# Performance work log

Hardware: AMD Instinct MI355X
Metric: run time of the kernel (lower is better)

The kernel has to match this reference:

```python
import jax, jax.numpy as jnp
import numpy as np

B, S, VOCAB, E, H, T = 256, 512, 50000, 256, 256, 32
PAD = VOCAB - 1  # mask = sentences != vocab_size - 1 in the original


def setup_inputs() -> dict:
    key = jax.random.key(0)
    ks = jax.random.split(key, 16)
    lengths = jnp.sort(jax.random.randint(ks[0], (B,), S // 2, S + 1))[::-1]
    lengths = lengths.at[0].set(S)  # sorted descending, max length present
    sentences = jax.random.randint(ks[1], (B, S), 0, VOCAB - 1)
    pos = jnp.arange(S)
    sentences = jnp.where(pos[None, :] < lengths[:, None], sentences, PAD)
    tags = jax.random.randint(ks[2], (B, S), 0, T)
    sc = jnp.float32(0.1)
    p = lambda k, shp: jax.random.normal(k, shp, jnp.float32) * sc
    return {
        'embed_table': p(ks[3], (VOCAB + 1, E)),
        'W_ih_f': p(ks[4], (4 * H, E)), 'W_hh_f': p(ks[5], (4 * H, H)),
        'b_ih_f': p(ks[6], (4 * H,)), 'b_hh_f': p(ks[7], (4 * H,)),
        'W_ih_b': p(ks[8], (4 * H, E)), 'W_hh_b': p(ks[9], (4 * H, H)),
        'b_ih_b': p(ks[10], (4 * H,)), 'b_hh_b': p(ks[11], (4 * H,)),
        'W_out': p(ks[12], (T, 2 * H)), 'b_out': p(ks[13], (T,)),
        'transition': jax.random.normal(ks[14], (T, T), jnp.float32),
        'sentences': sentences, 'tags': tags, 'sen_lengths': lengths,
    }


def _run_lstm(x_sbe, W_ih, W_hh, b_ih, b_hh):
    # x_sbe: [S, B, E]; torch gate order i, f, g, o
    Bsz, Hd = x_sbe.shape[1], W_hh.shape[1]
    gx = jnp.einsum('sbe,ge->sbg', x_sbe, W_ih) + b_ih + b_hh  # precompute input gates
    def step(carry, g):
        h, c = carry
        g = g + h @ W_hh.T
        i, f, gg, o = jnp.split(g, 4, axis=-1)
        c = jax.nn.sigmoid(f) * c + jax.nn.sigmoid(i) * jnp.tanh(gg)
        h = jax.nn.sigmoid(o) * jnp.tanh(c)
        return (h, c), h
    h0 = jnp.zeros((Bsz, Hd), x_sbe.dtype)
    _, hs = jax.lax.scan(step, (h0, h0), gx)
    return hs  # [S, B, H]


def _forward(embed_table, W_ih_f, W_hh_f, b_ih_f, b_hh_f,
             W_ih_b, W_hh_b, b_ih_b, b_hh_b, W_out, b_out, transition,
             sentences, tags, sen_lengths):
    mask = sentences != PAD                      # [B, S]
    x = embed_table[sentences]                   # [B, S, E]
    pos = jnp.arange(S)
    valid = pos[None, :] < sen_lengths[:, None]  # [B, S]
    # per-sequence reversal index (packed-sequence-faithful backward direction)
    idx = jnp.where(valid, sen_lengths[:, None] - 1 - pos[None, :], pos[None, :])
    h_f = _run_lstm(x.transpose(1, 0, 2), W_ih_f, W_hh_f, b_ih_f, b_hh_f).transpose(1, 0, 2)
    x_rev = jnp.take_along_axis(x, idx[:, :, None], axis=1)
    h_b = _run_lstm(x_rev.transpose(1, 0, 2), W_ih_b, W_hh_b, b_ih_b, b_hh_b).transpose(1, 0, 2)
    h_b = jnp.take_along_axis(h_b, idx[:, :, None], axis=1)
    h = jnp.concatenate([h_f, h_b], -1) * valid[:, :, None]  # pad_packed pads with zeros
    emit = h @ W_out.T + b_out                   # [B, S, T]; dropout is identity (eval)
    # ---- CRF negative log-likelihood ----
    fmask = mask.astype(emit.dtype)
    real = jnp.take_along_axis(emit, tags[:, :, None], axis=2)[..., 0]  # [B, S]
    real = real.at[:, 1:].add(transition[tags[:, :-1], tags[:, 1:]])
    real_score = (real * fmask).sum(axis=1)      # [B]
    def crf_step(alpha, inp):
        e_i, m_i = inp                           # [B, T], [B]
        scores = alpha[:, :, None] + transition[None, :, :] + e_i[:, None, :]
        new = jax.nn.logsumexp(scores, axis=1)
        return jnp.where(m_i[:, None], new, alpha), None
    alpha0 = emit[:, 0]                          # [B, T]
    xs = (emit[:, 1:].transpose(1, 0, 2), mask[:, 1:].T)
    alpha, _ = jax.lax.scan(crf_step, alpha0, xs)
    log_z = jax.nn.logsumexp(alpha, axis=1)      # [B]
    return -(real_score - log_z)                 # per-example loss [B]


def reference(embed_table, W_ih_f, W_hh_f, b_ih_f, b_hh_f,
              W_ih_b, W_hh_b, b_ih_b, b_hh_b, W_out, b_out, transition,
              sentences, tags, sen_lengths):
    return _forward(embed_table, W_ih_f, W_hh_f, b_ih_f, b_hh_f,
                    W_ih_b, W_hh_b, b_ih_b, b_hh_b, W_out, b_out, transition,
                    sentences, tags, sen_lengths)
```

## Files before the change

### kernel.cpp

```cpp
#include <hip/hip_runtime.h>
#include <hip/hip_bf16.h>


typedef __bf16 bf16x8 __attribute__((ext_vector_type(8)));
typedef float f32x4 __attribute__((ext_vector_type(4)));
typedef unsigned int uint4v __attribute__((ext_vector_type(4)));

__device__ __forceinline__ unsigned short f2bf(float f) {
  union { float f; unsigned int u; } v; v.f = f;
  unsigned int r = v.u + 0x7fffu + ((v.u >> 16) & 1u);
  return (unsigned short)(r >> 16);
}
__device__ __forceinline__ float bf2f(unsigned int lo16) {
  union { unsigned int u; float f; } v; v.u = lo16 << 16;
  return v.f;
}
__device__ __forceinline__ float fsig(float x) {
  float e = __builtin_amdgcn_exp2f(-1.4426950408889634f * x);
  return __builtin_amdgcn_rcpf(1.0f + e);
}
__device__ __forceinline__ float ftanh(float x) {
  float e = __builtin_amdgcn_exp2f(2.8853900817779268f * x);
  return 1.0f - 2.0f * __builtin_amdgcn_rcpf(e + 1.0f);
}

__device__ __forceinline__ void wait_ge(int* p, int target) {
  if (threadIdx.x == 0) {
    while (__hip_atomic_load(p, __ATOMIC_RELAXED, __HIP_MEMORY_SCOPE_AGENT) < target)
      __builtin_amdgcn_s_sleep(2);
    (void)__hip_atomic_load(p, __ATOMIC_ACQUIRE, __HIP_MEMORY_SCOPE_AGENT);
  }
  __syncthreads();
}

__global__ void cvt_weights(const float* __restrict__ wih_f, const float* __restrict__ wih_b,
                            const float* __restrict__ whh_f, const float* __restrict__ whh_b,
                            const float* __restrict__ wo,
                            unsigned short* __restrict__ wih,
                            unsigned char* __restrict__ whh8,
                            unsigned char* __restrict__ wout8,
                            int* __restrict__ flags) {
  if (blockIdx.x == 0 && threadIdx.x < 32) flags[threadIdx.x] = 0;
  int t = blockIdx.x * 256 + threadIdx.x;
  int i = t * 4;
  if (i < 524288) {
    const float* src = (i < 262144) ? wih_f : wih_b;
    f32x4 v = *(const f32x4*)(src + (i & 262143));
    uint2 p;
    p.x = f2bf(v[0]) | ((unsigned int)f2bf(v[1]) << 16);
    p.y = f2bf(v[2]) | ((unsigned int)f2bf(v[3]) << 16);
    *(uint2*)(wih + i) = p;
  } else if (i < 1048576) {
    int k = i - 524288;
    const float* src = (k < 262144) ? whh_f : whh_b;
    f32x4 v = *(const f32x4*)(src + (k & 262143));
    int r = 0;
    r = __builtin_amdgcn_cvt_pk_fp8_f32(v[0], v[1], r, false);
    r = __builtin_amdgcn_cvt_pk_fp8_f32(v[2], v[3], r, true);
    *(unsigned int*)(whh8 + k) = (unsigned int)r;
  } else if (i < 1064960) {
    int k = i - 1048576;
    f32x4 v = *(const f32x4*)(wo + k);
    int r = 0;
    r = __builtin_amdgcn_cvt_pk_fp8_f32(v[0], v[1], r, false);
    r = __builtin_amdgcn_cvt_pk_fp8_f32(v[2], v[3], r, true);
    *(unsigned int*)(wout8 + k) = (unsigned int)r;
  }
}


__device__ void gemm_role(
    const float* __restrict__ emb, const int* __restrict__ sent, const int* __restrict__ lens,
    const unsigned short* __restrict__ wih,
    const float* __restrict__ bih_f, const float* __restrict__ bhh_f,
    const float* __restrict__ bih_b, const float* __restrict__ bhh_b,
    unsigned short* __restrict__ gx, int* flags,
    unsigned short* wtile, float* btile)
{
  int gb = blockIdx.x - 64;
  int tid = threadIdx.x, w = tid >> 6, lane = tid & 63, col = lane & 15, q = lane >> 4;
  int ns = w >> 2, cg = w & 3;
  int prev_chunk = -1;

  for (int idx = gb; idx < 4096; idx += 192) {
    int k = idx >> 8, t = idx & 255;
    if (k != prev_chunk) {
      prev_chunk = k;
      if (k >= 2) wait_ge(&flags[16 + k - 2], 64);
    }
    int dir = t >> 7, r = t & 127;
    int nc = r >> 4, bt = (r >> 2) & 3, ss = r & 3;
    int n0 = nc * 128, bbase = bt * 64;
    int s0 = k * 32, sbase = s0 + ss * 8;

    if (sbase < lens[bbase]) {
      const unsigned short* wsrc = wih + (size_t)dir * 262144;
#pragma unroll
      for (int it = 0; it < 8; it++) {
        int seg = it * 512 + tid;
        int row = seg >> 5, kc = (seg & 31) * 8;
        *(uint4v*)(wtile + row * 264 + kc) = *(const uint4v*)(wsrc + (size_t)(n0 + row) * 256 + kc);
      }
      const float* bi = dir ? bih_b : bih_f;
      const float* bh = dir ? bhh_b : bhh_f;
      if (tid < 128) btile[tid] = bi[n0 + tid] + bh[n0 + tid];
      __syncthreads();

      bf16x8 wf[8][4];
#pragma unroll
      for (int kt = 0; kt < 8; kt++)
#pragma unroll
        for (int nt = 0; nt < 4; nt++)
          wf[kt][nt] = *(const bf16x8*)(wtile + (ns * 64 + nt * 16 + col) * 264 + kt * 32 + q * 8);
      f32x4 bias[4];
#pragma unroll
      for (int nt = 0; nt < 4; nt++)
#pragma unroll
        for (int rr = 0; rr < 4; rr++)
          bias[nt][rr] = btile[ns * 64 + nt * 16 + q * 4 + rr];

      int bidx = bbase + cg * 16 + col;
      int len = lens[bidx];
      const int* srow = sent + bidx * 512;

      for (int i = 0; i < 8; i++) {
        int s = sbase + i;
        int s_eff = dir ? ((s < len) ? (len - 1 - s) : s) : s;
        int token = srow[s_eff];
        const float* ep = emb + (size_t)token * 256;
        bf16x8 xf[8];
#pragma unroll
        for (int kt = 0; kt < 8; kt++) {
          f32x4 a0 = *(const f32x4*)(ep + kt * 32 + q * 8);
          f32x4 a1 = *(const f32x4*)(ep + kt * 32 + q * 8 + 4);
          uint4v pk;
          pk[0] = f2bf(a0[0]) | ((unsigned int)f2bf(a0[1]) << 16);
          pk[1] = f2bf(a0[2]) | ((unsigned int)f2bf(a0[3]) << 16);
          pk[2] = f2bf(a1[0]) | ((unsigned int)f2bf(a1[1]) << 16);
          pk[3] = f2bf(a1[2]) | ((unsigned int)f2bf(a1[3]) << 16);
          xf[kt] = __builtin_bit_cast(bf16x8, pk);
        }
        f32x4 acc[4];
#pragma unroll
        for (int nt = 0; nt < 4; nt++) acc[nt] = bias[nt];
#pragma unroll
        for (int kt = 0; kt < 8; kt++)
#pragma unroll
          for (int nt = 0; nt < 4; nt++)
            acc[nt] = __builtin_amdgcn_mfma_f32_16x16x32_bf16(wf[kt][nt], xf[kt], acc[nt], 0, 0, 0);
        size_t off = (size_t)(k & 1) * 16777216 + (size_t)dir * 8388608
                   + (size_t)(s - s0) * 262144 + (size_t)bidx * 1024 + n0 + ns * 64;
#pragma unroll
        for (int nt = 0; nt < 4; nt++) {
          uint2 pk;
          pk.x = f2bf(acc[nt][0]) | ((unsigned int)f2bf(acc[nt][1]) << 16);
          pk.y = f2bf(acc[nt][2]) | ((unsigned int)f2bf(acc[nt][3]) << 16);
          *(uint2*)(gx + off + nt * 16 + q * 4) = pk;
        }
      }
    }
    __syncthreads();
    if (tid == 0)
      __hip_atomic_fetch_add(&flags[k], 1, __ATOMIC_RELEASE, __HIP_MEMORY_SCOPE_AGENT);
  }
}

__device__ void lstm_role(
    const unsigned short* __restrict__ gx,
    const unsigned char* __restrict__ whh8,
    const unsigned char* __restrict__ wout8,
    const float* __restrict__ bout,
    const int* __restrict__ lens,
    unsigned short* __restrict__ emit_f, unsigned short* __restrict__ emit_b,
    int* flags, unsigned char (*hb4)[16 * 264])
{
  int bx = blockIdx.x;
  int dir = bx & 1, grp = bx >> 1, b0 = grp * 8;
  int tid = threadIdx.x, w = tid >> 6, lane = tid & 63, col = lane & 15, q = lane >> 4;
  int maxlen = lens[b0];
  int bcl = b0 + col; if (bcl > 255) bcl = 255;
  int mylen = lens[bcl];

  const unsigned char* whb = whh8 + (size_t)dir * 262144;
  long wh[8][8];
#pragma unroll
  for (int kt = 0; kt < 8; kt++)
#pragma unroll
    for (int t = 0; t < 8; t++) {
      int row0 = (t & 3) * 256 + w * 32 + (t >> 2) * 16;
      wh[kt][t] = *(const long*)(whb + (size_t)(row0 + col) * 256 + kt * 32 + q * 8);
    }

  long wo8[8];
  f32x4 bo4 = (f32x4){0.f, 0.f, 0.f, 0.f};
#pragma unroll
  for (int kt = 0; kt < 8; kt++)
    wo8[kt] = *(const long*)(wout8 + (size_t)((w & 1) * 16 + col) * 512 + dir * 256 + kt * 32 + q * 8);
  if (dir == 0) {
#pragma unroll
    for (int r = 0; r < 4; r++) bo4[r] = bout[(w & 1) * 16 + q * 4 + r];
  }
  unsigned short* ebase = dir ? emit_b : emit_f;

  float c8[8];
  long hf8[8];
#pragma unroll
  for (int i = 0; i < 8; i++) { c8[i] = 0.f; hf8[i] = 0; }

  for (int c = 0; c < 16; c++) {
    int s0 = c * 32;
    if (s0 < maxlen) {
      wait_ge(&flags[c], 256);
      int send = s0 + 32; if (send > maxlen) send = maxlen;
      const unsigned short* gl = gx + (size_t)(c & 1) * 16777216 + (size_t)dir * 8388608
                                    + (size_t)bcl * 1024 + q * 4;
      uint2 gxr[8];
#pragma unroll
      for (int t = 0; t < 8; t++) {
        int row0 = (t & 3) * 256 + w * 32 + (t >> 2) * 16;
        gxr[t] = *(const uint2*)(gl + row0);
      }

      for (int s = s0; s < send; s++) {
        f32x4 acc[8];
#pragma unroll
        for (int t = 0; t < 8; t++) {
          f32x4 a;
          a[0] = bf2f(gxr[t].x & 0xffffu); a[1] = bf2f(gxr[t].x >> 16);
          a[2] = bf2f(gxr[t].y & 0xffffu); a[3] = bf2f(gxr[t].y >> 16);
          acc[t] = a;
        }
        {
          int snl = (s + 1 < send) ? (s + 1 - s0) : (send - 1 - s0);
          const unsigned short* gn = gl + (size_t)snl * 262144;
#pragma unroll
          for (int t = 0; t < 8; t++) {
            int row0 = (t & 3) * 256 + w * 32 + (t >> 2) * 16;
            gxr[t] = *(const uint2*)(gn + row0);
          }
        }
#pragma unroll
        for (int kt = 0; kt < 8; kt++) {
          long hv8 = hf8[kt];
#pragma unroll
          for (int t = 0; t < 8; t++)
            acc[t] = __builtin_amdgcn_mfma_f32_16x16x32_fp8_fp8(wh[kt][t], hv8, acc[t], 0, 0, 0);
        }
        float hv[8];
#pragma unroll
        for (int a = 0; a < 2; a++)
#pragma unroll
          for (int r = 0; r < 4; r++) {
            float ig = acc[a * 4 + 0][r], fg = acc[a * 4 + 1][r];
            float gg = acc[a * 4 + 2][r], og = acc[a * 4 + 3][r];
            float cn = fsig(fg) * c8[a * 4 + r] + fsig(ig) * ftanh(gg);
            c8[a * 4 + r] = cn;
            hv[a * 4 + r] = fsig(og) * ftanh(cn);
          }
        int par = s & 7;
#pragma unroll
        for (int a = 0; a < 2; a++) {
          int r8 = 0;
          r8 = __builtin_amdgcn_cvt_pk_fp8_f32(hv[a * 4 + 0], hv[a * 4 + 1], r8, false);
          r8 = __builtin_amdgcn_cvt_pk_fp8_f32(hv[a * 4 + 2], hv[a * 4 + 3], r8, true);
          *(unsigned int*)(&hb4[par][col * 264 + w * 32 + a * 16 + q * 4]) = (unsigned int)r8;
        }
        __syncthreads();
#pragma unroll
        for (int kt = 0; kt < 8; kt++)
          hf8[kt] = *(const long*)(&hb4[par][col * 264 + kt * 32 + q * 8]);

        if ((s & 3) == 3 || s == send - 1) {
          int ebeg = s & ~3;
          int e = ebeg + (w >> 1);
          if (e <= s) {
            f32x4 ea = bo4;
#pragma unroll
            for (int kt = 0; kt < 8; kt++) {
              long hbv = *(const long*)(&hb4[e & 7][col * 264 + kt * 32 + q * 8]);
              ea = __builtin_amdgcn_mfma_f32_16x16x32_fp8_fp8(wo8[kt], hbv, ea, 0, 0, 0);
            }
            if (col < 8 && e < mylen) {
              int pos = dir ? (mylen - 1 - e) : e;
              uint2 pk;
              pk.x = f2bf(ea[0]) | ((unsigned int)f2bf(ea[1]) << 16);
              pk.y = f2bf(ea[2]) | ((unsigned int)f2bf(ea[3]) << 16);
              *(uint2*)(ebase + (((size_t)(b0 + col) * 512 + pos) * 32 + (w & 1) * 16 + q * 4)) = pk;
            }
          }
        }
      }
    }
    __syncthreads();
    if (tid == 0)
      __hip_atomic_fetch_add(&flags[16 + c], 1, __ATOMIC_RELEASE, __HIP_MEMORY_SCOPE_AGENT);
  }
}

__global__ __launch_bounds__(512, 2) void fused_persist(
    const float* __restrict__ emb, const int* __restrict__ sent, const int* __restrict__ lens,
    const unsigned short* __restrict__ wih,
    const float* __restrict__ bih_f, const float* __restrict__ bhh_f,
    const float* __restrict__ bih_b, const float* __restrict__ bhh_b,
    unsigned short* __restrict__ gx,
    const unsigned char* __restrict__ whh8, const unsigned char* __restrict__ wout8,
    const float* __restrict__ bout,
    unsigned short* __restrict__ emit_f, unsigned short* __restrict__ emit_b,
    int* flags)
{
  __shared__ __align__(16) unsigned short wtile[128 * 264];
  __shared__ __align__(16) float btile[128];
  __shared__ __align__(16) unsigned char hb4[8][16 * 264];

  if (blockIdx.x < 64) {
    lstm_role(gx, whh8, wout8, bout, lens, emit_f, emit_b, flags, hb4);
  } else {
    gemm_role(emb, sent, lens, wih, bih_f, bhh_f, bih_b, bhh_b, gx, flags, wtile, btile);
  }
}

__global__ __launch_bounds__(64) void crf_kernel(
    const unsigned short* __restrict__ emit_f,
    const unsigned short* __restrict__ emit_b,
    const float* __restrict__ trans, const int* __restrict__ tags,
    const int* __restrict__ lens, float* __restrict__ out) {
  const float LOG2E = 1.4426950408889634f, LN2 = 0.6931471805599453f;
  __shared__ __align__(16) float e_lds[512 * 32];
  int b = blockIdx.x, lane = threadIdx.x;
  int len = lens[b];
  const int* tg = tags + b * 512;

  size_t ebase = (size_t)b * 512 * 32;
  const unsigned short* pf = emit_f + ebase;
  const unsigned short* pb = emit_b + ebase;
  int ng = len * 4;
  for (int g = lane; g < ng; g += 64) {
    uint4v fv = *(const uint4v*)(pf + g * 8);
    uint4v bv = *(const uint4v*)(pb + g * 8);
    f32x4 w0, w1;
#pragma unroll
    for (int k = 0; k < 2; k++) {
      w0[2 * k]     = (bf2f(fv[k] & 0xffffu) + bf2f(bv[k] & 0xffffu)) * LOG2E;
      w0[2 * k + 1] = (bf2f(fv[k] >> 16)     + bf2f(bv[k] >> 16))     * LOG2E;
      w1[2 * k]     = (bf2f(fv[k + 2] & 0xffffu) + bf2f(bv[k + 2] & 0xffffu)) * LOG2E;
      w1[2 * k + 1] = (bf2f(fv[k + 2] >> 16)     + bf2f(bv[k + 2] >> 16))     * LOG2E;
    }
    *(f32x4*)(e_lds + g * 8) = w0;
    *(f32x4*)(e_lds + g * 8 + 4) = w1;
  }
  __syncthreads();

  float rs2 = 0.f, rst = 0.f;
  for (int s = lane; s < len; s += 64) {
    int t1 = tg[s];
    rs2 += e_lds[s * 32 + t1];
    if (s > 0) rst += trans[tg[s - 1] * 32 + t1];
  }
  float rsc = LN2 * rs2 + rst;
#pragma unroll
  for (int m = 32; m; m >>= 1) rsc += __shfl_xor(rsc, m);

  int j = lane & 31, half = lane >> 5, i0 = half * 16;
  float tr2[16];
  int pidx[16];
#pragma unroll
  for (int ii = 0; ii < 16; ii++) {
    tr2[ii] = trans[(i0 + ii) * 32 + j] * LOG2E;
    pidx[ii] = (i0 + ii) << 2;
  }
  const float* ep = e_lds + j;
  float B = ep[0];
  float e_nxt = ep[32];
  for (int s = 1; s < len; s++) {
    float e_cur = e_nxt;
    int sn = (s + 1 < len) ? (s + 1) : s;
    e_nxt = ep[sn * 32];
    float v[16];
#pragma unroll
    for (int ii = 0; ii < 16; ii++)
      v[ii] = __builtin_bit_cast(float, __builtin_amdgcn_ds_bpermute(
                  pidx[ii], __builtin_bit_cast(int, B))) + tr2[ii];
    float a8[8], a4[4], a2[2];
#pragma unroll
    for (int ii = 0; ii < 8; ii++) a8[ii] = fmaxf(v[ii], v[ii + 8]);
#pragma unroll
    for (int ii = 0; ii < 4; ii++) a4[ii] = fmaxf(a8[ii], a8[ii + 4]);
    a2[0] = fmaxf(a4[0], a4[2]); a2[1] = fmaxf(a4[1], a4[3]);
    float m1 = fmaxf(a2[0], a2[1]);
    float m2 = fmaxf(m1, __shfl_xor(m1, 32));
    float x[16];
#pragma unroll
    for (int ii = 0; ii < 16; ii++) x[ii] = __builtin_amdgcn_exp2f(v[ii] - m2);
    float s8[8], s4[4], s2[2];
#pragma unroll
    for (int ii = 0; ii < 8; ii++) s8[ii] = x[ii] + x[ii + 8];
#pragma unroll
    for (int ii = 0; ii < 4; ii++) s4[ii] = s8[ii] + s8[ii + 4];
    s2[0] = s4[0] + s4[2]; s2[1] = s4[1] + s4[3];
    float sum = s2[0] + s2[1];
    sum += __shfl_xor(sum, 32);
    B = m2 + __builtin_amdgcn_logf(sum) + e_cur;
  }
  float mz = B;
#pragma unroll
  for (int m = 16; m; m >>= 1) mz = fmaxf(mz, __shfl_xor(mz, m));
  float sz = __builtin_amdgcn_exp2f(B - mz);
#pragma unroll
  for (int m = 16; m; m >>= 1) sz += __shfl_xor(sz, m);
  float logz = LN2 * (mz + __builtin_amdgcn_logf(sz));
  if (lane == 0) out[b] = logz - rsc;
}

extern "C" void kernel_launch(void* const* d_in, const int* in_sizes, int n_in,
                              void* d_out, int out_size, void* d_ws, size_t ws_size,
                              hipStream_t stream) {
  const float* emb   = (const float*)d_in[0];
  const float* Wih_f = (const float*)d_in[1];
  const float* Whh_f = (const float*)d_in[2];
  const float* bih_f = (const float*)d_in[3];
  const float* bhh_f = (const float*)d_in[4];
  const float* Wih_b = (const float*)d_in[5];
  const float* Whh_b = (const float*)d_in[6];
  const float* bih_b = (const float*)d_in[7];
  const float* bhh_b = (const float*)d_in[8];
  const float* Wout  = (const float*)d_in[9];
  const float* bout  = (const float*)d_in[10];
  const float* trans = (const float*)d_in[11];
  const int* sent = (const int*)d_in[12];
  const int* tags = (const int*)d_in[13];
  const int* lens = (const int*)d_in[14];
  float* out = (float*)d_out;

  char* ws = (char*)d_ws;
  if (ws_size < 87048192ull) return;
  unsigned short* gx      = (unsigned short*)(ws);
  unsigned short* emit_f  = (unsigned short*)(ws + 67108864);
  unsigned short* emit_b  = (unsigned short*)(ws + 75497472);
  unsigned short* wih_bf  = (unsigned short*)(ws + 83886080);
  unsigned char*  whh8    = (unsigned char*)(ws + 84934656);
  unsigned char*  wout8   = (unsigned char*)(ws + 85458944);
  int*            flags   = (int*)(ws + 85475328);

  cvt_weights<<<1040, 256, 0, stream>>>(Wih_f, Wih_b, Whh_f, Whh_b, Wout,
                                        wih_bf, whh8, wout8, flags);
  fused_persist<<<256, 512, 0, stream>>>(
      emb, sent, lens, wih_bf, bih_f, bhh_f, bih_b, bhh_b, gx,
      whh8, wout8, bout, emit_f, emit_b, flags);
  crf_kernel<<<256, 64, 0, stream>>>(emit_f, emit_b, trans, tags, lens, out);
}
```

Before: 1.735 ms.

## Use 16-sequence LSTM blocks with fine-grained per-subchunk producer flags

LSTM blocks now each handle 16 sequences instead of 8, so half as many blocks (32) run the recurrence and more blocks (224) run the input-projection GEMM. The single per-chunk ready flag is replaced by flags per 8-step subchunk, direction and batch tile, so the recurrence can start as soon as its own slice of gx is written. The per-step __syncthreads is replaced by an explicit lgkmcnt wait plus s_barrier. This risks a longer serial recurrence per block, since each block now does twice the columns, and puts more polling traffic on the flags.

```diff
diff --git a/kernel.cpp b/kernel.cpp
--- a/kernel.cpp
+++ b/kernel.cpp
@@ -31,6 +31,10 @@
     (void)__hip_atomic_load(p, __ATOMIC_ACQUIRE, __HIP_MEMORY_SCOPE_AGENT);
   }
   __syncthreads();
+}
+
+__device__ __forceinline__ void lds_barrier() {
+  asm volatile("s_waitcnt lgkmcnt(0)\n\ts_barrier" ::: "memory");
 }
 
 __global__ void cvt_weights(const float* __restrict__ wih_f, const float* __restrict__ wih_b,
@@ -40,7 +44,9 @@
                             unsigned char* __restrict__ whh8,
                             unsigned char* __restrict__ wout8,
                             int* __restrict__ flags) {
-  if (blockIdx.x == 0 && threadIdx.x < 32) flags[threadIdx.x] = 0;
+  if (blockIdx.x == 0) {
+    for (int f = threadIdx.x; f < 544; f += 256) flags[f] = 0;
+  }
   int t = blockIdx.x * 256 + threadIdx.x;
   int i = t * 4;
   if (i < 524288) {
@@ -77,21 +83,21 @@
     unsigned short* __restrict__ gx, int* flags,
     unsigned short* wtile, float* btile)
 {
-  int gb = blockIdx.x - 64;
+  int gb = blockIdx.x - 32;
   int tid = threadIdx.x, w = tid >> 6, lane = tid & 63, col = lane & 15, q = lane >> 4;
   int ns = w >> 2, cg = w & 3;
   int prev_chunk = -1;
 
-  for (int idx = gb; idx < 4096; idx += 192) {
+  for (int idx = gb; idx < 4096; idx += 224) {
     int k = idx >> 8, t = idx & 255;
+    int ss = t >> 6, rest = t & 63;
+    int dir = (rest >> 5) & 1, nc = (rest >> 2) & 7, bt = rest & 3;
     if (k != prev_chunk) {
       prev_chunk = k;
-      if (k >= 2) wait_ge(&flags[16 + k - 2], 64);
+      if (k >= 2) wait_ge(&flags[512 + k - 2], 32);
     }
-    int dir = t >> 7, r = t & 127;
-    int nc = r >> 4, bt = (r >> 2) & 3, ss = r & 3;
     int n0 = nc * 128, bbase = bt * 64;
-    int s0 = k * 32, sbase = s0 + ss * 8;
+    int sbase = k * 32 + ss * 8;
 
     if (sbase < lens[bbase]) {
       const unsigned short* wsrc = wih + (size_t)dir * 262144;
@@ -149,7 +155,7 @@
           for (int nt = 0; nt < 4; nt++)
             acc[nt] = __builtin_amdgcn_mfma_f32_16x16x32_bf16(wf[kt][nt], xf[kt], acc[nt], 0, 0, 0);
         size_t off = (size_t)(k & 1) * 16777216 + (size_t)dir * 8388608
-                   + (size_t)(s - s0) * 262144 + (size_t)bidx * 1024 + n0 + ns * 64;
+                   + (size_t)(s - k * 32) * 262144 + (size_t)bidx * 1024 + n0 + ns * 64;
 #pragma unroll
         for (int nt = 0; nt < 4; nt++) {
           uint2 pk;
@@ -161,7 +167,8 @@
     }
     __syncthreads();
     if (tid == 0)
-      __hip_atomic_fetch_add(&flags[k], 1, __ATOMIC_RELEASE, __HIP_MEMORY_SCOPE_AGENT);
+      __hip_atomic_fetch_add(&flags[k * 32 + ss * 8 + dir * 4 + bt], 1,
+                             __ATOMIC_RELEASE, __HIP_MEMORY_SCOPE_AGENT);
   }
 }
 
@@ -175,10 +182,11 @@
     int* flags, unsigned char (*hb4)[16 * 264])
 {
   int bx = blockIdx.x;
-  int dir = bx & 1, grp = bx >> 1, b0 = grp * 8;
+  int dir = bx & 1, grp = bx >> 1, b0 = grp * 16;
+  int bt = grp >> 2;
   int tid = threadIdx.x, w = tid >> 6, lane = tid & 63, col = lane & 15, q = lane >> 4;
   int maxlen = lens[b0];
-  int bcl = b0 + col; if (bcl > 255) bcl = 255;
+  int bcl = b0 + col;
   int mylen = lens[bcl];
 
   const unsigned char* whb = whh8 + (size_t)dir * 262144;
@@ -210,82 +218,90 @@
   for (int c = 0; c < 16; c++) {
     int s0 = c * 32;
     if (s0 < maxlen) {
-      wait_ge(&flags[c], 256);
-      int send = s0 + 32; if (send > maxlen) send = maxlen;
-      const unsigned short* gl = gx + (size_t)(c & 1) * 16777216 + (size_t)dir * 8388608
-                                    + (size_t)bcl * 1024 + q * 4;
-      uint2 gxr[8];
-#pragma unroll
-      for (int t = 0; t < 8; t++) {
-        int row0 = (t & 3) * 256 + w * 32 + (t >> 2) * 16;
-        gxr[t] = *(const uint2*)(gl + row0);
-      }
-
-      for (int s = s0; s < send; s++) {
-        f32x4 acc[8];
-#pragma unroll
-        for (int t = 0; t < 8; t++) {
-          f32x4 a;
-          a[0] = bf2f(gxr[t].x & 0xffffu); a[1] = bf2f(gxr[t].x >> 16);
-          a[2] = bf2f(gxr[t].y & 0xffffu); a[3] = bf2f(gxr[t].y >> 16);
-          acc[t] = a;
-        }
+      int cend = s0 + 32; if (cend > maxlen) cend = maxlen;
+      const unsigned short* gbase = gx + (size_t)(c & 1) * 16777216 + (size_t)dir * 8388608
+                                       + (size_t)bcl * 1024 + q * 4;
+      for (int ss = 0; ss < 4; ss++) {
+        int sp0 = s0 + ss * 8;
+        if (sp0 >= maxlen) break;
+        int spe = sp0 + 8; if (spe > cend) spe = cend;
+        wait_ge(&flags[c * 32 + ss * 8 + dir * 4 + bt], 8);
+
+        uint2 gxr[8];
         {
-          int snl = (s + 1 < send) ? (s + 1 - s0) : (send - 1 - s0);
-          const unsigned short* gn = gl + (size_t)snl * 262144;
+          const unsigned short* gf = gbase + (size_t)(sp0 - s0) * 262144;
 #pragma unroll
           for (int t = 0; t < 8; t++) {
             int row0 = (t & 3) * 256 + w * 32 + (t >> 2) * 16;
-            gxr[t] = *(const uint2*)(gn + row0);
+            gxr[t] = *(const uint2*)(gf + row0);
           }
         }
-#pragma unroll
-        for (int kt = 0; kt < 8; kt++) {
-          long hv8 = hf8[kt];
-#pragma unroll
-          for (int t = 0; t < 8; t++)
-            acc[t] = __builtin_amdgcn_mfma_f32_16x16x32_fp8_fp8(wh[kt][t], hv8, acc[t], 0, 0, 0);
-        }
-        float hv[8];
-#pragma unroll
-        for (int a = 0; a < 2; a++)
-#pragma unroll
-          for (int r = 0; r < 4; r++) {
-            float ig = acc[a * 4 + 0][r], fg = acc[a * 4 + 1][r];
-            float gg = acc[a * 4 + 2][r], og = acc[a * 4 + 3][r];
-            float cn = fsig(fg) * c8[a * 4 + r] + fsig(ig) * ftanh(gg);
-            c8[a * 4 + r] = cn;
-            hv[a * 4 + r] = fsig(og) * ftanh(cn);
-          }
-        int par = s & 7;
-#pragma unroll
-        for (int a = 0; a < 2; a++) {
-          int r8 = 0;
-          r8 = __builtin_amdgcn_cvt_pk_fp8_f32(hv[a * 4 + 0], hv[a * 4 + 1], r8, false);
-          r8 = __builtin_amdgcn_cvt_pk_fp8_f32(hv[a * 4 + 2], hv[a * 4 + 3], r8, true);
-          *(unsigned int*)(&hb4[par][col * 264 + w * 32 + a * 16 + q * 4]) = (unsigned int)r8;
-        }
-        __syncthreads();
-#pragma unroll
-        for (int kt = 0; kt < 8; kt++)
-          hf8[kt] = *(const long*)(&hb4[par][col * 264 + kt * 32 + q * 8]);
-
-        if ((s & 3) == 3 || s == send - 1) {
-          int ebeg = s & ~3;
-          int e = ebeg + (w >> 1);
-          if (e <= s) {
-            f32x4 ea = bo4;
-#pragma unroll
-            for (int kt = 0; kt < 8; kt++) {
-              long hbv = *(const long*)(&hb4[e & 7][col * 264 + kt * 32 + q * 8]);
-              ea = __builtin_amdgcn_mfma_f32_16x16x32_fp8_fp8(wo8[kt], hbv, ea, 0, 0, 0);
+
+        for (int s = sp0; s < spe; s++) {
+          f32x4 acc[8];
+#pragma unroll
+          for (int t = 0; t < 8; t++) {
+            f32x4 a;
+            a[0] = bf2f(gxr[t].x & 0xffffu); a[1] = bf2f(gxr[t].x >> 16);
+            a[2] = bf2f(gxr[t].y & 0xffffu); a[3] = bf2f(gxr[t].y >> 16);
+            acc[t] = a;
+          }
+          if (s + 1 < spe) {
+            const unsigned short* gn = gbase + (size_t)(s + 1 - s0) * 262144;
+#pragma unroll
+            for (int t = 0; t < 8; t++) {
+              int row0 = (t & 3) * 256 + w * 32 + (t >> 2) * 16;
+              gxr[t] = *(const uint2*)(gn + row0);
             }
-            if (col < 8 && e < mylen) {
-              int pos = dir ? (mylen - 1 - e) : e;
-              uint2 pk;
-              pk.x = f2bf(ea[0]) | ((unsigned int)f2bf(ea[1]) << 16);
-              pk.y = f2bf(ea[2]) | ((unsigned int)f2bf(ea[3]) << 16);
-              *(uint2*)(ebase + (((size_t)(b0 + col) * 512 + pos) * 32 + (w & 1) * 16 + q * 4)) = pk;
+          }
+#pragma unroll
+          for (int kt = 0; kt < 8; kt++) {
+            long hv8 = hf8[kt];
+#pragma unroll
+            for (int t = 0; t < 8; t++)
+              acc[t] = __builtin_amdgcn_mfma_f32_16x16x32_fp8_fp8(wh[kt][t], hv8, acc[t], 0, 0, 0);
+          }
+          float hv[8];
+#pragma unroll
+          for (int a = 0; a < 2; a++)
+#pragma unroll
+            for (int r = 0; r < 4; r++) {
+              float ig = acc[a * 4 + 0][r], fg = acc[a * 4 + 1][r];
+              float gg = acc[a * 4 + 2][r], og = acc[a * 4 + 3][r];
+              float cn = fsig(fg) * c8[a * 4 + r] + fsig(ig) * ftanh(gg);
+              c8[a * 4 + r] = cn;
+              hv[a * 4 + r] = fsig(og) * ftanh(cn);
+            }
+          int par = s & 7;
+#pragma unroll
+          for (int a = 0; a < 2; a++) {
+            int r8 = 0;
+            r8 = __builtin_amdgcn_cvt_pk_fp8_f32(hv[a * 4 + 0], hv[a * 4 + 1], r8, false);
+            r8 = __builtin_amdgcn_cvt_pk_fp8_f32(hv[a * 4 + 2], hv[a * 4 + 3], r8, true);
+            *(unsigned int*)(&hb4[par][col * 264 + w * 32 + a * 16 + q * 4]) = (unsigned int)r8;
+          }
+          lds_barrier();
+#pragma unroll
+          for (int kt = 0; kt < 8; kt++)
+            hf8[kt] = *(const long*)(&hb4[par][col * 264 + kt * 32 + q * 8]);
+
+          if ((s & 3) == 3 || s == spe - 1) {
+            int ebeg = s & ~3;
+            int e = ebeg + (w >> 1);
+            if (e <= s) {
+              f32x4 ea = bo4;
+#pragma unroll
+              for (int kt = 0; kt < 8; kt++) {
+                long hbv = *(const long*)(&hb4[e & 7][col * 264 + kt * 32 + q * 8]);
+                ea = __builtin_amdgcn_mfma_f32_16x16x32_fp8_fp8(wo8[kt], hbv, ea, 0, 0, 0);
+              }
+              if (e < mylen) {
+                int pos = dir ? (mylen - 1 - e) : e;
+                uint2 pk;
+                pk.x = f2bf(ea[0]) | ((unsigned int)f2bf(ea[1]) << 16);
+                pk.y = f2bf(ea[2]) | ((unsigned int)f2bf(ea[3]) << 16);
+                *(uint2*)(ebase + (((size_t)bcl * 512 + pos) * 32 + (w & 1) * 16 + q * 4)) = pk;
+              }
             }
           }
         }
@@ -293,7 +309,7 @@
     }
     __syncthreads();
     if (tid == 0)
-      __hip_atomic_fetch_add(&flags[16 + c], 1, __ATOMIC_RELEASE, __HIP_MEMORY_SCOPE_AGENT);
+      __hip_atomic_fetch_add(&flags[512 + c], 1, __ATOMIC_RELEASE, __HIP_MEMORY_SCOPE_AGENT);
   }
 }
 
@@ -312,7 +328,7 @@
   __shared__ __align__(16) float btile[128];
   __shared__ __align__(16) unsigned char hb4[8][16 * 264];
 
-  if (blockIdx.x < 64) {
+  if (blockIdx.x < 32) {
     lstm_role(gx, whh8, wout8, bout, lens, emit_f, emit_b, flags, hb4);
   } else {
     gemm_role(emb, sent, lens, wih, bih_f, bhh_f, bih_b, bhh_b, gx, flags, wtile, btile);
```

Result: faster. 1.545 ms (-10.9%).
